# Kernel optimization log

Hardware: AMD Instinct MI355X
Metric: run time of the kernel (lower is better)

The kernel has to match this reference:

```python
import jax, jax.numpy as jnp
import numpy as np

NUM_HEADS = 16
ROPE_BASE = 10000.0


def _rope_cos_sin(seq_len, head_dim, dtype):
    # freqs for the half-dim; original caches cat(freqs, freqs) and then applies
    # the rotation per-half, which is equivalent to using the half-size tables.
    inv_freq = 1.0 / (ROPE_BASE ** (jnp.arange(0, head_dim, 2, dtype=jnp.float32) / head_dim))
    t = jnp.arange(seq_len, dtype=jnp.float32)
    freqs = jnp.einsum('i,j->ij', t, inv_freq)  # [S, hd/2]
    return jnp.cos(freqs).astype(dtype), jnp.sin(freqs).astype(dtype)


def _apply_rotary(x, cos, sin):
    # x: [B, H, S, hd]; cos/sin: [S, hd/2] broadcast over B, H
    half = x.shape[-1] // 2
    x1, x2 = x[..., :half], x[..., half:]
    return jnp.concatenate([x1 * cos - x2 * sin, x2 * cos + x1 * sin], axis=-1)


def setup_inputs() -> dict:
    key = jax.random.key(0)
    ks = jax.random.split(key, 5)
    D = 2048
    B, S = 2, 2048
    std = 1.0 / np.sqrt(D)
    return {
        'x': jax.random.normal(ks[0], (B, S, D), dtype=jnp.float32),
        'Wq': jax.random.normal(ks[1], (D, D), dtype=jnp.float32) * std,
        'Wk': jax.random.normal(ks[2], (D, D), dtype=jnp.float32) * std,
        'Wv': jax.random.normal(ks[3], (D, D), dtype=jnp.float32) * std,
        'Wo': jax.random.normal(ks[4], (D, D), dtype=jnp.float32) * std,
    }


def reference(x, Wq, Wk, Wv, Wo):
    B, S, D = x.shape
    H = NUM_HEADS
    hd = D // H
    scale = hd ** -0.5

    def proj(W):  # torch Linear: y = x @ W.T -> [B, H, S, hd]
        return (x @ W.T).reshape(B, S, H, hd).transpose(0, 2, 1, 3)

    q, k, v = proj(Wq), proj(Wk), proj(Wv)

    cos, sin = _rope_cos_sin(S, hd, x.dtype)
    q = _apply_rotary(q, cos, sin)
    k = _apply_rotary(k, cos, sin)

    scores = jnp.einsum('bhqd,bhkd->bhqk', q, k) * scale  # full O(S^2) scores
    attn = jax.nn.softmax(scores, axis=-1)
    out = jnp.einsum('bhqk,bhkd->bhqd', attn, v)
    out = out.transpose(0, 2, 1, 3).reshape(B, S, D)
    return out @ Wo.T
```

## Files before the change

### kernel.cpp

```cpp
#include <hip/hip_runtime.h>
#include <cstdint>

typedef __attribute__((ext_vector_type(8))) short bf16x8;
typedef __attribute__((ext_vector_type(4))) float f32x4;
typedef __attribute__((ext_vector_type(16))) float f32x16;

__device__ inline unsigned short f2bf(float f) {
  uint32_t u = __float_as_uint(f);
  uint32_t lsb = (u >> 16) & 1u;
  u += 0x7fffu + lsb;
  return (unsigned short)(u >> 16);
}
__device__ inline float bf2f(unsigned short b) {
  return __uint_as_float(((uint32_t)b) << 16);
}
__device__ inline uint32_t cvt_pk_bf16(float lo, float hi) {
  uint32_t r;
  asm volatile("v_cvt_pk_bf16_f32 %0, %1, %2" : "=v"(r) : "v"(lo), "v"(hi));
  return r;
}

#define GLOAD16(gp, lp)                                                        \
  __builtin_amdgcn_global_load_lds(                                            \
      (const __attribute__((address_space(1))) void*)(gp),                     \
      (__attribute__((address_space(3))) void*)(lp), 16, 0, 0)

__global__ void cvt_f32_bf16(const float* __restrict__ in,
                             unsigned short* __restrict__ out, int n) {
  int i = (blockIdx.x * 256 + threadIdx.x) * 4;
  if (i >= n) return;
  float4 v = *(const float4*)(in + i);
  unsigned short o[4] = {f2bf(v.x), f2bf(v.y), f2bf(v.z), f2bf(v.w)};
  *(uint64_t*)(out + i) = *(const uint64_t*)o;
}

__global__ void rope_table_k(float* __restrict__ ctab, float* __restrict__ stab) {
  int i = blockIdx.x * 256 + threadIdx.x;
  int s = i >> 6, j = i & 63;
  float invf = expf(-(float)j * (9.210340371976184f / 64.0f));
  float ang = (float)s * invf;
  ctab[i] = cosf(ang);
  stab[i] = sinf(ang);
}

__global__ void rope_apply_k(unsigned short* __restrict__ qb,
                             unsigned short* __restrict__ kb,
                             const float* __restrict__ ctab,
                             const float* __restrict__ stab) {
  int row = blockIdx.x * 4 + (threadIdx.x >> 6);
  int t = threadIdx.x & 63;
  int s = row & 2047;
  int bh = (row >> 11) & 31;
  int isK = row >> 16;
  unsigned short* base = isK ? kb : qb;
  float qs = isK ? 1.0f : (0.08838834764831845f * 1.4426950408889634f);
  unsigned short* p = base + ((size_t)bh * 2048 + s) * 128;
  float c = ctab[s * 64 + t], sn = stab[s * 64 + t];
  float x1 = bf2f(p[t]), x2 = bf2f(p[t + 64]);
  p[t] = f2bf((x1 * c - x2 * sn) * qs);
  p[t + 64] = f2bf((x2 * c + x1 * sn) * qs);
}

__global__ void transpose_v_k(const unsigned short* __restrict__ v,
                              unsigned short* __restrict__ vt) {
  __shared__ unsigned short tile[64][72];
  int bh = blockIdx.x, st = blockIdx.y, dt = blockIdx.z;
  const unsigned short* src = v + ((size_t)bh * 2048 + st * 64) * 128 + dt * 64;
  unsigned short* dst = vt + ((size_t)bh * 128 + dt * 64) * 2048 + st * 64;
  int t = threadIdx.x;
  int r = t >> 2, c0 = (t & 3) * 16;
  *(bf16x8*)&tile[r][c0] = *(const bf16x8*)(src + (size_t)r * 128 + c0);
  *(bf16x8*)&tile[r][c0 + 8] = *(const bf16x8*)(src + (size_t)r * 128 + c0 + 8);
  __syncthreads();
  unsigned short o[16];
#pragma unroll
  for (int i = 0; i < 16; i++) o[i] = tile[c0 + i][r];
  *(bf16x8*)(dst + (size_t)r * 2048 + c0) = *(const bf16x8*)&o[0];
  *(bf16x8*)(dst + (size_t)r * 2048 + c0 + 8) = *(const bf16x8*)&o[8];
}

template <int EPI>
__global__ __launch_bounds__(256, 2) void gemm_bt(
    const unsigned short* __restrict__ A, const unsigned short* __restrict__ Bm,
    float* __restrict__ Cf, unsigned short* __restrict__ q_out,
    unsigned short* __restrict__ k_out, unsigned short* __restrict__ v_out,
    int M, int N, int K) {
  __shared__ unsigned short sA[128 * 32];
  __shared__ unsigned short sB[128 * 32];
  const int t = threadIdx.x;
  const int w = t >> 6, l = t & 63;
  const int wr = w >> 1, wc = w & 1;
  const int bm = blockIdx.x * 128, bn = blockIdx.y * 128;
  const int lr = l & 15, lg = l >> 4;
  f32x4 acc[4][4] = {};

  const int srow = w * 16 + (l >> 2);
  const int sseg = (l & 3) * 8;
  const unsigned short* ga = A + (size_t)(bm + srow) * K + sseg;
  const unsigned short* gb = Bm + (size_t)(bn + srow) * K + sseg;
  unsigned short* lA = sA + w * 512 + l * 8;
  unsigned short* lB = sB + w * 512 + l * 8;

  for (int kt = 0; kt < K; kt += 32) {
    __syncthreads();
    GLOAD16(ga + kt, lA);
    GLOAD16(ga + kt + (size_t)64 * K, lA + 2048);
    GLOAD16(gb + kt, lB);
    GLOAD16(gb + kt + (size_t)64 * K, lB + 2048);
    __syncthreads();
    bf16x8 af[4], bfv[4];
#pragma unroll
    for (int m = 0; m < 4; m++)
      af[m] = *(const bf16x8*)(sA + (wr * 64 + m * 16 + lr) * 32 + lg * 8);
#pragma unroll
    for (int n = 0; n < 4; n++)
      bfv[n] = *(const bf16x8*)(sB + (wc * 64 + n * 16 + lr) * 32 + lg * 8);
#pragma unroll
    for (int m = 0; m < 4; m++)
#pragma unroll
      for (int n = 0; n < 4; n++)
        acc[m][n] = __builtin_amdgcn_mfma_f32_16x16x32_bf16(af[m], bfv[n],
                                                            acc[m][n], 0, 0, 0);
  }

#pragma unroll
  for (int m = 0; m < 4; m++) {
#pragma unroll
    for (int n = 0; n < 4; n++) {
      int gm0 = bm + wr * 64 + m * 16 + lg * 4;
      int gn = bn + wc * 64 + n * 16 + lr;
#pragma unroll
      for (int j = 0; j < 4; j++) {
        float v = acc[m][n][j];
        int gm = gm0 + j;
        if (EPI == 0) {
          Cf[(size_t)gm * N + gn] = v;
        } else {
          int which = gn >> 11, rem = gn & 2047;
          int h = rem >> 7, d = rem & 127;
          int b = gm >> 11, s = gm & 2047;
          unsigned short* dst = which == 0 ? q_out : (which == 1 ? k_out : v_out);
          dst[(((size_t)(b * 16 + h)) * 2048 + s) * 128 + d] = f2bf(v);
        }
      }
    }
  }
}

template <int EPI>
__global__ __launch_bounds__(512, 1) void gemm256(
    const unsigned short* __restrict__ A, const unsigned short* __restrict__ Bm,
    float* __restrict__ Cf, unsigned short* __restrict__ q_out,
    unsigned short* __restrict__ k_out, unsigned short* __restrict__ v_out,
    int M, int N, int K, int nbm) {
  __shared__ unsigned short sA[2][2][256 * 32];
  __shared__ unsigned short sB[2][2][256 * 32];

  const int t = threadIdx.x;
  const int w = t >> 6, l = t & 63;
  const int wr = w >> 2, wc = w & 3;
  const int lr = l & 15, lg = l >> 4;
  const int gsw = (lg ^ (lr & 3)) * 8;

  const int cpx = gridDim.x >> 3;
  const int bid = blockIdx.x;
  const int swz = (bid & 7) * cpx + (bid >> 3);
  const int bm = (swz % nbm) * 256, bn = (swz / nbm) * 256;

  f32x4 acc[8][4] = {};

  int rowi[2], goff[2];
#pragma unroll
  for (int i = 0; i < 2; i++) {
    int idx = i * 512 + t;
    rowi[i] = idx >> 2;
    goff[i] = ((idx & 3) ^ (rowi[i] & 3)) * 8;
  }
  const unsigned short* Ab = A + (size_t)bm * K;
  const unsigned short* Bb = Bm + (size_t)bn * K;

#define STAGE256(Xb, plane, koff)                                              \
  do {                                                                         \
    _Pragma("unroll") for (int i = 0; i < 2; i++)                              \
        GLOAD16(Xb + (size_t)rowi[i] * K + (koff) + goff[i],                   \
                (plane) + (i * 512 + t) * 8);                                  \
  } while (0)

  STAGE256(Ab, sA[0][0], 0);
  STAGE256(Bb, sB[0][0], 0);
  STAGE256(Ab, sA[0][1], 32);
  STAGE256(Bb, sB[0][1], 32);
  asm volatile("s_waitcnt vmcnt(4)" ::: "memory");
  __builtin_amdgcn_s_barrier();

  const int NT = K >> 6;
  for (int t2 = 0; t2 < NT; ++t2) {
    const int db = t2 & 1, dn = db ^ 1;
    const int kt = (t2 + 1 < NT ? t2 + 1 : t2) * 64;
    bf16x8 a[4], a2[4], b[4];

#pragma unroll
    for (int mf = 0; mf < 4; mf++)
      a[mf] = *(const bf16x8*)&sA[db][0][(wr * 128 + mf * 16 + lr) * 32 + gsw];
#pragma unroll
    for (int nf = 0; nf < 4; nf++)
      b[nf] = *(const bf16x8*)&sB[db][0][(wc * 64 + nf * 16 + lr) * 32 + gsw];
    STAGE256(Ab, sA[dn][0], kt);
    __builtin_amdgcn_s_barrier();
    asm volatile("s_waitcnt lgkmcnt(0)" ::: "memory");
    __builtin_amdgcn_sched_barrier(0);
    __builtin_amdgcn_s_setprio(1);
#pragma unroll
    for (int mf = 0; mf < 4; mf++)
#pragma unroll
      for (int nf = 0; nf < 4; nf++)
        acc[mf][nf] = __builtin_amdgcn_mfma_f32_16x16x32_bf16(a[mf], b[nf],
                                                              acc[mf][nf], 0, 0, 0);
    __builtin_amdgcn_s_setprio(0);
    __builtin_amdgcn_s_barrier();

#pragma unroll
    for (int mf = 0; mf < 4; mf++)
      a2[mf] = *(const bf16x8*)&sA[db][0][(wr * 128 + (mf + 4) * 16 + lr) * 32 + gsw];
    STAGE256(Bb, sB[dn][0], kt);
    __builtin_amdgcn_s_barrier();
    asm volatile("s_waitcnt lgkmcnt(0)" ::: "memory");
    __builtin_amdgcn_sched_barrier(0);
    __builtin_amdgcn_s_setprio(1);
#pragma unroll
    for (int mf = 0; mf < 4; mf++)
#pragma unroll
      for (int nf = 0; nf < 4; nf++)
        acc[mf + 4][nf] = __builtin_amdgcn_mfma_f32_16x16x32_bf16(
            a2[mf], b[nf], acc[mf + 4][nf], 0, 0, 0);
    __builtin_amdgcn_s_setprio(0);
    asm volatile("s_waitcnt vmcnt(4)" ::: "memory");
    __builtin_amdgcn_s_barrier();

#pragma unroll
    for (int mf = 0; mf < 4; mf++)
      a[mf] = *(const bf16x8*)&sA[db][1][(wr * 128 + mf * 16 + lr) * 32 + gsw];
#pragma unroll
    for (int nf = 0; nf < 4; nf++)
      b[nf] = *(const bf16x8*)&sB[db][1][(wc * 64 + nf * 16 + lr) * 32 + gsw];
    STAGE256(Ab, sA[dn][1], kt + 32);
    __builtin_amdgcn_s_barrier();
    asm volatile("s_waitcnt lgkmcnt(0)" ::: "memory");
    __builtin_amdgcn_sched_barrier(0);
    __builtin_amdgcn_s_setprio(1);
#pragma unroll
    for (int mf = 0; mf < 4; mf++)
#pragma unroll
      for (int nf = 0; nf < 4; nf++)
        acc[mf][nf] = __builtin_amdgcn_mfma_f32_16x16x32_bf16(a[mf], b[nf],
                                                              acc[mf][nf], 0, 0, 0);
    __builtin_amdgcn_s_setprio(0);
    __builtin_amdgcn_s_barrier();

#pragma unroll
    for (int mf = 0; mf < 4; mf++)
      a2[mf] = *(const bf16x8*)&sA[db][1][(wr * 128 + (mf + 4) * 16 + lr) * 32 + gsw];
    STAGE256(Bb, sB[dn][1], kt + 32);
    __builtin_amdgcn_s_barrier();
    asm volatile("s_waitcnt lgkmcnt(0)" ::: "memory");
    __builtin_amdgcn_sched_barrier(0);
    __builtin_amdgcn_s_setprio(1);
#pragma unroll
    for (int mf = 0; mf < 4; mf++)
#pragma unroll
      for (int nf = 0; nf < 4; nf++)
        acc[mf + 4][nf] = __builtin_amdgcn_mfma_f32_16x16x32_bf16(
            a2[mf], b[nf], acc[mf + 4][nf], 0, 0, 0);
    __builtin_amdgcn_s_setprio(0);
    asm volatile("s_waitcnt vmcnt(4)" ::: "memory");
    __builtin_amdgcn_s_barrier();
  }

#pragma unroll
  for (int mf = 0; mf < 8; mf++) {
#pragma unroll
    for (int nf = 0; nf < 4; nf++) {
      int gm0 = bm + wr * 128 + mf * 16 + lg * 4;
      int gn = bn + wc * 64 + nf * 16 + lr;
#pragma unroll
      for (int j = 0; j < 4; j++) {
        float v = acc[mf][nf][j];
        int gm = gm0 + j;
        if (EPI == 0) {
          Cf[(size_t)gm * N + gn] = v;
        } else {
          int which = gn >> 11, rem = gn & 2047;
          int h = rem >> 7, d = rem & 127;
          int b = gm >> 11, s = gm & 2047;
          unsigned short* dst = which == 0 ? q_out : (which == 1 ? k_out : v_out);
          dst[(((size_t)(b * 16 + h)) * 2048 + s) * 128 + d] = f2bf(v);
        }
      }
    }
  }
}

__global__ __launch_bounds__(256, 2) void attn_k(
    const unsigned short* __restrict__ Q, const unsigned short* __restrict__ K,
    const unsigned short* __restrict__ Vt, unsigned short* __restrict__ ctx) {
  __shared__ unsigned short sK[2][64 * 128];
  __shared__ unsigned short sV[2][128 * 64];

  const int qt = blockIdx.x, bh = blockIdx.y;
  const int t = threadIdx.x;
  const int w = t >> 6, l = t & 63;
  const int lq = l & 31;
  const int h5 = l >> 5;
  const int b = bh >> 4, hh = bh & 15;
  const int q0 = qt * 128 + w * 32;
  const unsigned short* Qp = Q + ((size_t)bh * 2048 + q0) * 128;
  const unsigned short* Kbh = K + (size_t)bh * 2048 * 128;
  const unsigned short* Vbh = Vt + (size_t)bh * 128 * 2048;

  int gko[4], gvo[4];
#pragma unroll
  for (int i = 0; i < 4; i++) {
    int p = i * 256 + t;
    int rK = p >> 4, cK = p & 15;
    gko[i] = rK * 128 + ((cK ^ (rK & 7)) * 8);
    int rV = p >> 3, cV = p & 7;
    gvo[i] = rV * 2048 + ((cV ^ (rV & 7)) * 8);
  }

  bf16x8 qf[8];
#pragma unroll
  for (int st = 0; st < 8; st++)
    qf[st] = *(const bf16x8*)(Qp + lq * 128 + st * 16 + h5 * 8);

  f32x16 o[4];
#pragma unroll
  for (int db = 0; db < 4; db++) o[db] = (f32x16)0.0f;
  float m_r = -1e30f, l_r = 0.0f;

#define STAGE_KV(buf, kv)                                                      \
  do {                                                                         \
    _Pragma("unroll") for (int i = 0; i < 4; i++)                              \
        GLOAD16(Kbh + (size_t)(kv)*128 + gko[i],                               \
                sK[buf] + (i * 256 + t) * 8);                                  \
    _Pragma("unroll") for (int i = 0; i < 4; i++)                              \
        GLOAD16(Vbh + (size_t)(kv) + gvo[i], sV[buf] + (i * 256 + t) * 8);     \
  } while (0)

  STAGE_KV(0, 0);
  __syncthreads();

  for (int it = 0; it < 32; ++it) {
    const int cur = it & 1;
    if (it < 31) STAGE_KV(cur ^ 1, (it + 1) * 64);

    const char* kbuf = (const char*)sK[cur];
    const char* vbuf = (const char*)sV[cur];

    f32x16 s2[2];
#pragma unroll
    for (int kb2 = 0; kb2 < 2; kb2++) {
      s2[kb2] = (f32x16)0.0f;
      const int rr = kb2 * 32 + lq;
      const int swzz = (rr & 7) << 4;
#pragma unroll
      for (int st = 0; st < 8; st++) {
        bf16x8 kf = *(const bf16x8*)(kbuf + rr * 256 + ((st * 32 + h5 * 16) ^ swzz));
        s2[kb2] = __builtin_amdgcn_mfma_f32_32x32x16_bf16(kf, qf[st], s2[kb2], 0, 0, 0);
      }
    }

    float sm[32];
#pragma unroll
    for (int kb2 = 0; kb2 < 2; kb2++)
#pragma unroll
      for (int r = 0; r < 16; r++) sm[kb2 * 16 + r] = s2[kb2][r];

    float tmax = sm[0];
#pragma unroll
    for (int i = 1; i < 32; i++) tmax = fmaxf(tmax, sm[i]);
    tmax = fmaxf(tmax, __shfl_xor(tmax, 32));

    if (!__all(tmax <= m_r + 8.0f)) {
      float m_new = fmaxf(m_r, tmax);
      float fac = exp2f(m_r - m_new);
      l_r *= fac;
      float fo[16];
#pragma unroll
      for (int r = 0; r < 16; r++)
        fo[r] = __shfl(fac, (r & 3) + 8 * (r >> 2) + 4 * h5);
#pragma unroll
      for (int db = 0; db < 4; db++)
#pragma unroll
        for (int r = 0; r < 16; r++) o[db][r] *= fo[r];
      m_r = m_new;
    }

    float psum = 0.0f;
#pragma unroll
    for (int i = 0; i < 32; i++) {
      sm[i] = exp2f(sm[i] - m_r);
      psum += sm[i];
    }
    psum += __shfl_xor(psum, 32);
    l_r += psum;

    uint32_t wAp[2][4], wBp[2][4];
#pragma unroll
    for (int kb2 = 0; kb2 < 2; kb2++)
#pragma unroll
      for (int rq = 0; rq < 4; rq++) {
        wAp[kb2][rq] = cvt_pk_bf16(sm[kb2 * 16 + rq * 4 + 0], sm[kb2 * 16 + rq * 4 + 1]);
        wBp[kb2][rq] = cvt_pk_bf16(sm[kb2 * 16 + rq * 4 + 2], sm[kb2 * 16 + rq * 4 + 3]);
      }

#pragma unroll
    for (int st = 0; st < 4; st++) {
      const int kb2 = st >> 1, p2 = (st & 1) * 2;
      uint32_t keepA = h5 ? wAp[kb2][p2 + 1] : wAp[kb2][p2];
      uint32_t keepB = h5 ? wBp[kb2][p2 + 1] : wBp[kb2][p2];
      uint32_t sendA = h5 ? wAp[kb2][p2] : wAp[kb2][p2 + 1];
      uint32_t sendB = h5 ? wBp[kb2][p2] : wBp[kb2][p2 + 1];
      uint32_t partA = __shfl_xor(sendA, 32);
      uint32_t partB = __shfl_xor(sendB, 32);
      union {
        uint32_t u[4];
        bf16x8 v;
      } pu;
      pu.u[0] = h5 ? partA : keepA;
      pu.u[1] = h5 ? partB : keepB;
      pu.u[2] = h5 ? keepA : partA;
      pu.u[3] = h5 ? keepB : partB;
#pragma unroll
      for (int db = 0; db < 4; db++) {
        const int rv = db * 32 + lq;
        const int swzz = (rv & 7) << 4;
        bf16x8 vb = *(const bf16x8*)(vbuf + rv * 128 + ((st * 32 + h5 * 16) ^ swzz));
        o[db] = __builtin_amdgcn_mfma_f32_32x32x16_bf16(pu.v, vb, o[db], 0, 0, 0);
      }
    }
    __syncthreads();
  }

  float inv = 1.0f / l_r;
  float io[16];
#pragma unroll
  for (int r = 0; r < 16; r++)
    io[r] = __shfl(inv, (r & 3) + 8 * (r >> 2) + 4 * h5);
#pragma unroll
  for (int db = 0; db < 4; db++) {
#pragma unroll
    for (int r = 0; r < 16; r++) {
      int s = q0 + (r & 3) + 8 * (r >> 2) + 4 * h5;
      ctx[((size_t)(b * 2048 + s)) * 2048 + hh * 128 + db * 32 + lq] =
          f2bf(o[db][r] * io[r]);
    }
  }
}

extern "C" void kernel_launch(void* const* d_in, const int* in_sizes, int n_in,
                              void* d_out, int out_size, void* d_ws,
                              size_t ws_size, hipStream_t stream) {
  const float* x = (const float*)d_in[0];
  const float* Wq = (const float*)d_in[1];
  const float* Wk = (const float*)d_in[2];
  const float* Wv = (const float*)d_in[3];
  const float* Wo = (const float*)d_in[4];
  float* out = (float*)d_out;

  const size_t BS = 4096;
  const size_t D = 2048;

  char* p = (char*)d_ws;
  unsigned short* xb = (unsigned short*)p;   p += BS * D * 2;
  unsigned short* wqkv = (unsigned short*)p; p += 3 * D * D * 2;
  unsigned short* wo = (unsigned short*)p;   p += D * D * 2;
  unsigned short* qb = (unsigned short*)p;   p += BS * D * 2;
  unsigned short* kb = (unsigned short*)p;   p += BS * D * 2;
  unsigned short* vb = (unsigned short*)p;   p += BS * D * 2;
  float* ctab = (float*)p;                   p += 2048 * 64 * 4;
  float* stab = (float*)p;                   p += 2048 * 64 * 4;
  unsigned short* vt = wqkv;
  unsigned short* ctx = xb;

  cvt_f32_bf16<<<8388608 / 1024, 256, 0, stream>>>(x, xb, 8388608);
  cvt_f32_bf16<<<4194304 / 1024, 256, 0, stream>>>(Wq, wqkv, 4194304);
  cvt_f32_bf16<<<4194304 / 1024, 256, 0, stream>>>(Wk, wqkv + 4194304, 4194304);
  cvt_f32_bf16<<<4194304 / 1024, 256, 0, stream>>>(Wv, wqkv + 8388608, 4194304);
  cvt_f32_bf16<<<4194304 / 1024, 256, 0, stream>>>(Wo, wo, 4194304);
  rope_table_k<<<131072 / 256, 256, 0, stream>>>(ctab, stab);

  gemm256<1><<<384, 512, 0, stream>>>(xb, wqkv, nullptr, qb, kb, vb, 4096, 6144,
                                      2048, 16);
  rope_apply_k<<<32768, 256, 0, stream>>>(qb, kb, ctab, stab);
  transpose_v_k<<<dim3(32, 32, 2), 256, 0, stream>>>(vb, vt);
  attn_k<<<dim3(16, 32), 256, 0, stream>>>(qb, kb, vt, ctx);
  gemm_bt<0><<<dim3(32, 16), 256, 0, stream>>>(ctx, wo, out, nullptr, nullptr,
                                               nullptr, 4096, 2048, 2048);
}
```

Before: 355.6 us.

## Fuse fp32-to-bf16 conversions, vectorize RoPE apply, change GEMM LDS swizzle

Merges the five separate fp32-to-bf16 conversion launches into one kernel that routes each element range to the correct source and destination, removing launch overhead. RoPE application now handles four elements per thread with 64-bit loads and stores instead of scalar 16-bit accesses, cutting instruction count and the number of memory transactions. The QKV GEMM's LDS XOR swizzle now keys on (row>>1)&3 instead of row&3, consistently on both the staging and read sides, to reduce LDS bank conflicts. The fused converter adds per-thread branching on the destination.

```diff
diff --git a/kernel.cpp b/kernel.cpp
--- a/kernel.cpp
+++ b/kernel.cpp
@@ -25,13 +25,29 @@
       (const __attribute__((address_space(1))) void*)(gp),                     \
       (__attribute__((address_space(3))) void*)(lp), 16, 0, 0)
 
-__global__ void cvt_f32_bf16(const float* __restrict__ in,
-                             unsigned short* __restrict__ out, int n) {
-  int i = (blockIdx.x * 256 + threadIdx.x) * 4;
-  if (i >= n) return;
-  float4 v = *(const float4*)(in + i);
+__global__ void cvt_all(const float* __restrict__ x, const float* __restrict__ wq,
+                        const float* __restrict__ wk, const float* __restrict__ wv,
+                        const float* __restrict__ wos, unsigned short* __restrict__ xb,
+                        unsigned short* __restrict__ wqkv,
+                        unsigned short* __restrict__ wo) {
+  size_t e = ((size_t)blockIdx.x * 256 + threadIdx.x) * 4;
+  const float* src;
+  unsigned short* dst;
+  if (e < 8388608) {
+    src = x + e;
+    dst = xb + e;
+  } else {
+    size_t r = e - 8388608;
+    int k = (int)(r >> 22);
+    size_t off = r & 4194303;
+    if (k == 0) { src = wq + off; dst = wqkv + r; }
+    else if (k == 1) { src = wk + off; dst = wqkv + r; }
+    else if (k == 2) { src = wv + off; dst = wqkv + r; }
+    else { src = wos + off; dst = wo + off; }
+  }
+  float4 v = *(const float4*)src;
   unsigned short o[4] = {f2bf(v.x), f2bf(v.y), f2bf(v.z), f2bf(v.w)};
-  *(uint64_t*)(out + i) = *(const uint64_t*)o;
+  *(uint64_t*)dst = *(const uint64_t*)o;
 }
 
 __global__ void rope_table_k(float* __restrict__ ctab, float* __restrict__ stab) {
@@ -47,18 +63,29 @@
                              unsigned short* __restrict__ kb,
                              const float* __restrict__ ctab,
                              const float* __restrict__ stab) {
-  int row = blockIdx.x * 4 + (threadIdx.x >> 6);
-  int t = threadIdx.x & 63;
+  int row = blockIdx.x * 16 + (threadIdx.x >> 4);
+  int c = (threadIdx.x & 15) * 4;
   int s = row & 2047;
   int bh = (row >> 11) & 31;
   int isK = row >> 16;
   unsigned short* base = isK ? kb : qb;
   float qs = isK ? 1.0f : (0.08838834764831845f * 1.4426950408889634f);
   unsigned short* p = base + ((size_t)bh * 2048 + s) * 128;
-  float c = ctab[s * 64 + t], sn = stab[s * 64 + t];
-  float x1 = bf2f(p[t]), x2 = bf2f(p[t + 64]);
-  p[t] = f2bf((x1 * c - x2 * sn) * qs);
-  p[t + 64] = f2bf((x2 * c + x1 * sn) * qs);
+  float4 cv = *(const float4*)(ctab + s * 64 + c);
+  float4 sv = *(const float4*)(stab + s * 64 + c);
+  union { unsigned short u[4]; uint64_t q; } a, b2, oa, ob;
+  a.q = *(const uint64_t*)(p + c);
+  b2.q = *(const uint64_t*)(p + 64 + c);
+  float cc[4] = {cv.x, cv.y, cv.z, cv.w};
+  float ss[4] = {sv.x, sv.y, sv.z, sv.w};
+#pragma unroll
+  for (int i = 0; i < 4; i++) {
+    float x1 = bf2f(a.u[i]), x2 = bf2f(b2.u[i]);
+    oa.u[i] = f2bf((x1 * cc[i] - x2 * ss[i]) * qs);
+    ob.u[i] = f2bf((x2 * cc[i] + x1 * ss[i]) * qs);
+  }
+  *(uint64_t*)(p + c) = oa.q;
+  *(uint64_t*)(p + 64 + c) = ob.q;
 }
 
 __global__ void transpose_v_k(const unsigned short* __restrict__ v,
@@ -160,7 +187,7 @@
   const int w = t >> 6, l = t & 63;
   const int wr = w >> 2, wc = w & 3;
   const int lr = l & 15, lg = l >> 4;
-  const int gsw = (lg ^ (lr & 3)) * 8;
+  const int gsw = (lg ^ ((lr >> 1) & 3)) * 8;
 
   const int cpx = gridDim.x >> 3;
   const int bid = blockIdx.x;
@@ -169,27 +196,23 @@
 
   f32x4 acc[8][4] = {};
 
-  int rowi[2], goff[2];
-#pragma unroll
-  for (int i = 0; i < 2; i++) {
-    int idx = i * 512 + t;
-    rowi[i] = idx >> 2;
-    goff[i] = ((idx & 3) ^ (rowi[i] & 3)) * 8;
-  }
   const unsigned short* Ab = A + (size_t)bm * K;
   const unsigned short* Bb = Bm + (size_t)bn * K;
 
-#define STAGE256(Xb, plane, koff)                                              \
+#define STAGE_H(Xb, plane, koff)                                               \
   do {                                                                         \
-    _Pragma("unroll") for (int i = 0; i < 2; i++)                              \
-        GLOAD16(Xb + (size_t)rowi[i] * K + (koff) + goff[i],                   \
-                (plane) + (i * 512 + t) * 8);                                  \
+    _Pragma("unroll") for (int i = 0; i < 2; i++) {                            \
+      int g = i * 512 + t;                                                     \
+      int row = g >> 2, c = g & 3;                                             \
+      GLOAD16(Xb + (size_t)row * K + (koff) + ((c ^ ((row >> 1) & 3)) * 8),    \
+              (plane) + g * 8);                                                \
+    }                                                                          \
   } while (0)
 
-  STAGE256(Ab, sA[0][0], 0);
-  STAGE256(Bb, sB[0][0], 0);
-  STAGE256(Ab, sA[0][1], 32);
-  STAGE256(Bb, sB[0][1], 32);
+  STAGE_H(Ab, &sA[0][0][0], 0);
+  STAGE_H(Bb, &sB[0][0][0], 0);
+  STAGE_H(Ab, &sA[0][1][0], 32);
+  STAGE_H(Bb, &sB[0][1][0], 32);
   asm volatile("s_waitcnt vmcnt(4)" ::: "memory");
   __builtin_amdgcn_s_barrier();
 
@@ -205,7 +228,7 @@
 #pragma unroll
     for (int nf = 0; nf < 4; nf++)
       b[nf] = *(const bf16x8*)&sB[db][0][(wc * 64 + nf * 16 + lr) * 32 + gsw];
-    STAGE256(Ab, sA[dn][0], kt);
+    STAGE_H(Ab, &sA[dn][0][0], kt);
     __builtin_amdgcn_s_barrier();
     asm volatile("s_waitcnt lgkmcnt(0)" ::: "memory");
     __builtin_amdgcn_sched_barrier(0);
@@ -222,7 +245,7 @@
 #pragma unroll
     for (int mf = 0; mf < 4; mf++)
       a2[mf] = *(const bf16x8*)&sA[db][0][(wr * 128 + (mf + 4) * 16 + lr) * 32 + gsw];
-    STAGE256(Bb, sB[dn][0], kt);
+    STAGE_H(Bb, &sB[dn][0][0], kt);
     __builtin_amdgcn_s_barrier();
     asm volatile("s_waitcnt lgkmcnt(0)" ::: "memory");
     __builtin_amdgcn_sched_barrier(0);
@@ -243,7 +266,7 @@
 #pragma unroll
     for (int nf = 0; nf < 4; nf++)
       b[nf] = *(const bf16x8*)&sB[db][1][(wc * 64 + nf * 16 + lr) * 32 + gsw];
-    STAGE256(Ab, sA[dn][1], kt + 32);
+    STAGE_H(Ab, &sA[dn][1][0], kt + 32);
     __builtin_amdgcn_s_barrier();
     asm volatile("s_waitcnt lgkmcnt(0)" ::: "memory");
     __builtin_amdgcn_sched_barrier(0);
@@ -260,7 +283,7 @@
 #pragma unroll
     for (int mf = 0; mf < 4; mf++)
       a2[mf] = *(const bf16x8*)&sA[db][1][(wr * 128 + (mf + 4) * 16 + lr) * 32 + gsw];
-    STAGE256(Bb, sB[dn][1], kt + 32);
+    STAGE_H(Bb, &sB[dn][1][0], kt + 32);
     __builtin_amdgcn_s_barrier();
     asm volatile("s_waitcnt lgkmcnt(0)" ::: "memory");
     __builtin_amdgcn_sched_barrier(0);
@@ -482,16 +505,12 @@
   unsigned short* vt = wqkv;
   unsigned short* ctx = xb;
 
-  cvt_f32_bf16<<<8388608 / 1024, 256, 0, stream>>>(x, xb, 8388608);
-  cvt_f32_bf16<<<4194304 / 1024, 256, 0, stream>>>(Wq, wqkv, 4194304);
-  cvt_f32_bf16<<<4194304 / 1024, 256, 0, stream>>>(Wk, wqkv + 4194304, 4194304);
-  cvt_f32_bf16<<<4194304 / 1024, 256, 0, stream>>>(Wv, wqkv + 8388608, 4194304);
-  cvt_f32_bf16<<<4194304 / 1024, 256, 0, stream>>>(Wo, wo, 4194304);
-  rope_table_k<<<131072 / 256, 256, 0, stream>>>(ctab, stab);
+  cvt_all<<<24576, 256, 0, stream>>>(x, Wq, Wk, Wv, Wo, xb, wqkv, wo);
+  rope_table_k<<<512, 256, 0, stream>>>(ctab, stab);
 
   gemm256<1><<<384, 512, 0, stream>>>(xb, wqkv, nullptr, qb, kb, vb, 4096, 6144,
                                       2048, 16);
-  rope_apply_k<<<32768, 256, 0, stream>>>(qb, kb, ctab, stab);
+  rope_apply_k<<<8192, 256, 0, stream>>>(qb, kb, ctab, stab);
   transpose_v_k<<<dim3(32, 32, 2), 256, 0, stream>>>(vb, vt);
   attn_k<<<dim3(16, 32), 256, 0, stream>>>(qb, kb, vt, ctx);
   gemm_bt<0><<<dim3(32, 16), 256, 0, stream>>>(ctx, wo, out, nullptr, nullptr,
```

Result: faster. 339.5 us (-4.5%).
